# Kernel tuning notes

Hardware: AMD Instinct MI355X
Metric: run time of the kernel (lower is better)

## Reference

```python
import jax, jax.numpy as jnp
import numpy as np


def setup_inputs() -> dict:
    key = jax.random.key(0)
    k1, k2 = jax.random.split(key)
    T, D, E = 8192, 4096, 64
    x = jax.random.normal(k1, (T, D), dtype=jnp.float32)
    gate_w = jax.random.normal(k2, (E, D), dtype=jnp.float32) * (1.0 / np.sqrt(D))
    return {"x": x, "gate_w": gate_w}


def reference(x, gate_w):
    TOPK = 8
    # logits = x @ W^T, computed in float32 like .float() in torch
    logits = jnp.einsum('td,ed->te', x, gate_w).astype(jnp.float32)
    scores = jax.nn.sigmoid(scores_in := logits) if False else jax.nn.sigmoid(logits)
    # top-k scores per token; values are exactly the gathered weights
    weights, indices = jax.lax.top_k(scores, TOPK)
    weights = weights / jnp.clip(jnp.sum(weights, axis=-1, keepdims=True), 1e-12)
    return weights.astype(x.dtype), indices
```

## Files before the change

### kernel.cpp

```cpp
#include <hip/hip_runtime.h>
#include <math.h>

#define T_TOTAL 8192
#define D_TOTAL 4096
#define E 64
#define TOPK 8
#define NKB (D_TOTAL / 32)

typedef short short8 __attribute__((ext_vector_type(8)));
typedef float f32x4 __attribute__((ext_vector_type(4)));

__device__ __forceinline__ void split3(const float* v8, short8& h, short8& m, short8& l) {
#pragma unroll
    for (int j = 0; j < 8; ++j) {
        const float f = v8[j];
        const unsigned u = __float_as_uint(f);
        const unsigned hu = u & 0xffff0000u;
        const float r1 = f - __uint_as_float(hu);
        const unsigned mu = __float_as_uint(r1) & 0xffff0000u;
        const float r2 = r1 - __uint_as_float(mu);
        const unsigned lu = __float_as_uint(r2);
        h[j] = (short)(hu >> 16);
        m[j] = (short)(mu >> 16);
        l[j] = (short)(lu >> 16);
    }
}

__device__ __forceinline__ void split3v(const float* v, short8& h, short8& m, short8& l) {
    unsigned* hp = reinterpret_cast<unsigned*>(&h);
    unsigned* mp = reinterpret_cast<unsigned*>(&m);
    unsigned* lp = reinterpret_cast<unsigned*>(&l);
#pragma unroll
    for (int p = 0; p < 4; ++p) {
        const float a = v[2 * p], b = v[2 * p + 1];
        const unsigned hw = __builtin_amdgcn_perm(__float_as_uint(b), __float_as_uint(a), 0x07060302u);
        const float r0 = a - __uint_as_float(hw << 16);
        const float r1 = b - __uint_as_float(hw & 0xffff0000u);
        const unsigned mw = __builtin_amdgcn_perm(__float_as_uint(r1), __float_as_uint(r0), 0x07060302u);
        const float s0 = r0 - __uint_as_float(mw << 16);
        const float s1 = r1 - __uint_as_float(mw & 0xffff0000u);
        const unsigned lw = __builtin_amdgcn_perm(__float_as_uint(s1), __float_as_uint(s0), 0x07060302u);
        hp[p] = hw; mp[p] = mw; lp[p] = lw;
    }
}

__global__ __launch_bounds__(256)
void prep_w(const float* __restrict__ w, short8* __restrict__ Bh,
            short8* __restrict__ Bm, short8* __restrict__ Bl) {
    const int t = blockIdx.x * 256 + threadIdx.x;
    const int lane = t & 63;
    const int nt = (t >> 6) & 3;
    const int kb = t >> 8;
    const int e = nt * 16 + (lane & 15);
    const int k = kb * 32 + (lane >> 4) * 8;

    const float* src = w + (size_t)e * D_TOTAL + k;
    float v[8];
    *reinterpret_cast<float4*>(&v[0]) = *reinterpret_cast<const float4*>(src);
    *reinterpret_cast<float4*>(&v[4]) = *reinterpret_cast<const float4*>(src + 4);

    short8 h, m, l;
    split3(v, h, m, l);
    Bh[t] = h; Bm[t] = m; Bl[t] = l;
}

__global__ __launch_bounds__(1024, 8)
void fused_router(const float* __restrict__ x,
                  const short8* __restrict__ Bh, const short8* __restrict__ Bm,
                  const short8* __restrict__ Bl,
                  float* __restrict__ out) {
    __shared__ float tiles[8 * 1024];
    __shared__ float fin[1024];

    const int tid = threadIdx.x;
    const int lane = tid & 63;
    const int wv = tid >> 6;
    const int tok0 = blockIdx.x * 16;

    const int row = lane & 15;
    const int kq = lane >> 4;

    const float* xb = x + (size_t)(tok0 + row) * D_TOTAL + kq * 8;

    f32x4 acc[4];
#pragma unroll
    for (int n = 0; n < 4; ++n) acc[n] = (f32x4){0.f, 0.f, 0.f, 0.f};

    const int kbase = wv * 256;

    float xr[8];
    {
        const float* ap = xb + kbase;
        *reinterpret_cast<float4*>(&xr[0]) = *reinterpret_cast<const float4*>(ap);
        *reinterpret_cast<float4*>(&xr[4]) = *reinterpret_cast<const float4*>(ap + 4);
    }

#pragma unroll
    for (int kb = 0; kb < 8; ++kb) {
        const int k = kbase + kb * 32;
        const int gkb = k >> 5;

        short8 ah, am_, al;
        split3v(xr, ah, am_, al);
        if (kb < 7) {
            const float* ap = xb + k + 32;
            *reinterpret_cast<float4*>(&xr[0]) = *reinterpret_cast<const float4*>(ap);
            *reinterpret_cast<float4*>(&xr[4]) = *reinterpret_cast<const float4*>(ap + 4);
        }

#pragma unroll
        for (int nt = 0; nt < 4; ++nt) {
            const size_t bi = (size_t)(gkb * 4 + nt) * 64 + lane;
            const short8 bh = Bh[bi];
            const short8 bm = Bm[bi];
            const short8 bl = Bl[bi];
            f32x4 c = acc[nt];
            c = __builtin_amdgcn_mfma_f32_16x16x32_bf16(ah,  bh, c, 0, 0, 0);
            c = __builtin_amdgcn_mfma_f32_16x16x32_bf16(ah,  bm, c, 0, 0, 0);
            c = __builtin_amdgcn_mfma_f32_16x16x32_bf16(am_, bh, c, 0, 0, 0);
            c = __builtin_amdgcn_mfma_f32_16x16x32_bf16(am_, bm, c, 0, 0, 0);
            c = __builtin_amdgcn_mfma_f32_16x16x32_bf16(ah,  bl, c, 0, 0, 0);
            c = __builtin_amdgcn_mfma_f32_16x16x32_bf16(al,  bh, c, 0, 0, 0);
            acc[nt] = c;
        }
    }

    if (wv >= 8) {
        float* s = &tiles[(size_t)(wv - 8) * 1024 + lane];
#pragma unroll
        for (int nt = 0; nt < 4; ++nt)
#pragma unroll
            for (int r = 0; r < 4; ++r)
                s[(nt * 4 + r) * 64] = acc[nt][r];
    }
    __syncthreads();
    if (wv < 8) {
        float* s = &tiles[(size_t)wv * 1024 + lane];
#pragma unroll
        for (int nt = 0; nt < 4; ++nt)
#pragma unroll
            for (int r = 0; r < 4; ++r) {
                const int j = (nt * 4 + r) * 64;
                s[j] = acc[nt][r] + s[j];
            }
    }
    __syncthreads();

    {
        float s0 = 0.f;
#pragma unroll
        for (int w2 = 0; w2 < 8; ++w2) s0 += tiles[w2 * 1024 + tid];
        const int j = tid >> 6, ln = tid & 63;
        const int t = (ln >> 4) * 4 + (j & 3);
        const int e = (j >> 2) * 16 + (ln & 15);
        fin[t * 64 + e] = s0;
    }
    __syncthreads();

    {
        const int t = wv;
        float v = fin[t * 64 + lane];
        float wj[TOPK];
        int   ij[TOPK];
        float wsum = 0.f;
#pragma unroll
        for (int j = 0; j < TOPK; ++j) {
            float mx = v;
#pragma unroll
            for (int off = 32; off >= 1; off >>= 1)
                mx = fmaxf(mx, __shfl_xor(mx, off));
            const unsigned long long msk = __ballot(v == mx);
            const int widx = (int)__builtin_ctzll(msk);
            wj[j] = 1.f / (1.f + expf(-mx));
            ij[j] = widx;
            wsum += wj[j];
            if (lane == widx) v = -INFINITY;
        }
        const float inv = 1.f / fmaxf(wsum, 1e-12f);
        const int tg = tok0 + t;
        if (lane == 0) {
#pragma unroll
            for (int j = 0; j < TOPK; ++j)
                out[(size_t)tg * TOPK + j] = wj[j] * inv;
#pragma unroll
            for (int j = 0; j < TOPK; ++j)
                out[(size_t)T_TOTAL * TOPK + (size_t)tg * TOPK + j] = (float)ij[j];
        }
    }
}

extern "C" void kernel_launch(void* const* d_in, const int* in_sizes, int n_in,
                              void* d_out, int out_size, void* d_ws, size_t ws_size,
                              hipStream_t stream) {
    const float* x = (const float*)d_in[0];
    const float* w = (const float*)d_in[1];
    float* out = (float*)d_out;

    short8* Bh = (short8*)d_ws;
    short8* Bm = Bh + (size_t)NKB * 4 * 64;
    short8* Bl = Bm + (size_t)NKB * 4 * 64;

    prep_w<<<NKB * 4 * 64 / 256, 256, 0, stream>>>(w, Bh, Bm, Bl);
    fused_router<<<T_TOTAL / 16, 1024, 0, stream>>>(x, Bh, Bm, Bl, out);
}
```

Before: 58.74 us.

## Split-K GEMM with LDS-staged weights and separate top-k reduction kernel

Replaces the fused per-16-token kernel with a split-K GEMM. Each block loads one K-chunk of the pre-split bf16 weight planes into LDS and reuses it across 256 tokens, with x loads triple-buffered. Partial logits are written to a workspace and then summed by a new top-k kernel that also runs sigmoid, selection and normalization. This cuts redundant global weight reads across token blocks, at the cost of an extra launch and about 32MB of partial-sum traffic.

```diff
diff --git a/kernel.cpp b/kernel.cpp
--- a/kernel.cpp
+++ b/kernel.cpp
@@ -6,6 +6,14 @@
 #define E 64
 #define TOPK 8
 #define NKB (D_TOTAL / 32)
+
+#define S_SPLIT 16
+#define KCH (D_TOTAL / S_SPLIT)
+#define KB_PER_BLK (KCH / 32)
+#define TOKW 16
+#define WVS 16
+#define TOKB (TOKW * WVS)
+#define CHUNK8 (KB_PER_BLK * 4 * 64)
 
 typedef short short8 __attribute__((ext_vector_type(8)));
 typedef float f32x4 __attribute__((ext_vector_type(4)));
@@ -64,101 +72,125 @@
     Bh[t] = h; Bm[t] = m; Bl[t] = l;
 }
 
-__global__ __launch_bounds__(1024, 8)
-void fused_router(const float* __restrict__ x,
-                  const short8* __restrict__ Bh, const short8* __restrict__ Bm,
-                  const short8* __restrict__ Bl,
-                  float* __restrict__ out) {
-    __shared__ float tiles[8 * 1024];
-    __shared__ float fin[1024];
+__global__ __launch_bounds__(1024, 4)
+void gemm_lds(const float* __restrict__ x,
+              const short8* __restrict__ Bh, const short8* __restrict__ Bm,
+              const short8* __restrict__ Bl,
+              float* __restrict__ part) {
+    __shared__ short8 Bs[3 * CHUNK8];
 
     const int tid = threadIdx.x;
     const int lane = tid & 63;
     const int wv = tid >> 6;
-    const int tok0 = blockIdx.x * 16;
+    const int s = blockIdx.y;
+    const int tok0 = blockIdx.x * TOKB + wv * TOKW;
+
+    {
+        const short8* g0 = Bh + (size_t)s * CHUNK8;
+        const short8* g1 = Bm + (size_t)s * CHUNK8;
+        const short8* g2 = Bl + (size_t)s * CHUNK8;
+#pragma unroll
+        for (int t = 0; t < 6; ++t) {
+            const int j = t * 1024 + tid;
+            const int a = j >> 11;
+            const int idx = j & (CHUNK8 - 1);
+            const short8* g = (a == 0) ? g0 : (a == 1) ? g1 : g2;
+            Bs[j] = g[idx];
+        }
+    }
 
     const int row = lane & 15;
     const int kq = lane >> 4;
-
-    const float* xb = x + (size_t)(tok0 + row) * D_TOTAL + kq * 8;
+    const float* xb = x + (size_t)(tok0 + row) * D_TOTAL + s * KCH + kq * 8;
 
     f32x4 acc[4];
 #pragma unroll
     for (int n = 0; n < 4; ++n) acc[n] = (f32x4){0.f, 0.f, 0.f, 0.f};
 
-    const int kbase = wv * 256;
-
-    float xr[8];
-    {
-        const float* ap = xb + kbase;
-        *reinterpret_cast<float4*>(&xr[0]) = *reinterpret_cast<const float4*>(ap);
-        *reinterpret_cast<float4*>(&xr[4]) = *reinterpret_cast<const float4*>(ap + 4);
-    }
-
-#pragma unroll
-    for (int kb = 0; kb < 8; ++kb) {
-        const int k = kbase + kb * 32;
-        const int gkb = k >> 5;
+    float xr[3][8];
+#pragma unroll
+    for (int p = 0; p < 2; ++p) {
+        const float* ap = xb + p * 32;
+        *reinterpret_cast<float4*>(&xr[p][0]) = *reinterpret_cast<const float4*>(ap);
+        *reinterpret_cast<float4*>(&xr[p][4]) = *reinterpret_cast<const float4*>(ap + 4);
+    }
+
+    __syncthreads();
+
+#pragma unroll
+    for (int kb = 0; kb < KB_PER_BLK; ++kb) {
+        if (kb < KB_PER_BLK - 2) {
+            const float* ap = xb + (kb + 2) * 32;
+            *reinterpret_cast<float4*>(&xr[(kb + 2) % 3][0]) = *reinterpret_cast<const float4*>(ap);
+            *reinterpret_cast<float4*>(&xr[(kb + 2) % 3][4]) = *reinterpret_cast<const float4*>(ap + 4);
+        }
 
         short8 ah, am_, al;
-        split3v(xr, ah, am_, al);
-        if (kb < 7) {
-            const float* ap = xb + k + 32;
-            *reinterpret_cast<float4*>(&xr[0]) = *reinterpret_cast<const float4*>(ap);
-            *reinterpret_cast<float4*>(&xr[4]) = *reinterpret_cast<const float4*>(ap + 4);
-        }
-
+        split3v(xr[kb % 3], ah, am_, al);
+
+        short8 bh[4], bm[4], bl[4];
 #pragma unroll
         for (int nt = 0; nt < 4; ++nt) {
-            const size_t bi = (size_t)(gkb * 4 + nt) * 64 + lane;
-            const short8 bh = Bh[bi];
-            const short8 bm = Bm[bi];
-            const short8 bl = Bl[bi];
+            const int bi = (kb * 4 + nt) * 64 + lane;
+            bh[nt] = Bs[bi];
+            bm[nt] = Bs[CHUNK8 + bi];
+            bl[nt] = Bs[2 * CHUNK8 + bi];
+        }
+
+#pragma unroll
+        for (int nt = 0; nt < 4; ++nt) {
             f32x4 c = acc[nt];
-            c = __builtin_amdgcn_mfma_f32_16x16x32_bf16(ah,  bh, c, 0, 0, 0);
-            c = __builtin_amdgcn_mfma_f32_16x16x32_bf16(ah,  bm, c, 0, 0, 0);
-            c = __builtin_amdgcn_mfma_f32_16x16x32_bf16(am_, bh, c, 0, 0, 0);
-            c = __builtin_amdgcn_mfma_f32_16x16x32_bf16(am_, bm, c, 0, 0, 0);
-            c = __builtin_amdgcn_mfma_f32_16x16x32_bf16(ah,  bl, c, 0, 0, 0);
-            c = __builtin_amdgcn_mfma_f32_16x16x32_bf16(al,  bh, c, 0, 0, 0);
+            c = __builtin_amdgcn_mfma_f32_16x16x32_bf16(ah,  bh[nt], c, 0, 0, 0);
+            c = __builtin_amdgcn_mfma_f32_16x16x32_bf16(ah,  bm[nt], c, 0, 0, 0);
+            c = __builtin_amdgcn_mfma_f32_16x16x32_bf16(am_, bh[nt], c, 0, 0, 0);
+            c = __builtin_amdgcn_mfma_f32_16x16x32_bf16(am_, bm[nt], c, 0, 0, 0);
+            c = __builtin_amdgcn_mfma_f32_16x16x32_bf16(ah,  bl[nt], c, 0, 0, 0);
+            c = __builtin_amdgcn_mfma_f32_16x16x32_bf16(al,  bh[nt], c, 0, 0, 0);
             acc[nt] = c;
         }
     }
 
-    if (wv >= 8) {
-        float* s = &tiles[(size_t)(wv - 8) * 1024 + lane];
-#pragma unroll
-        for (int nt = 0; nt < 4; ++nt)
-#pragma unroll
-            for (int r = 0; r < 4; ++r)
-                s[(nt * 4 + r) * 64] = acc[nt][r];
-    }
+    float* pb = part + ((size_t)s * T_TOTAL + tok0) * E;
+#pragma unroll
+    for (int nt = 0; nt < 4; ++nt) {
+        const int e = nt * 16 + (lane & 15);
+#pragma unroll
+        for (int r = 0; r < 4; ++r) {
+            const int t = (lane >> 4) * 4 + r;
+            pb[(size_t)t * E + e] = acc[nt][r];
+        }
+    }
+}
+
+__global__ __launch_bounds__(256)
+void topk_kernel(const float* __restrict__ part, float* __restrict__ out) {
+    __shared__ float fin[32 * 64];
+
+    const int tid = threadIdx.x;
+    const int tok0 = blockIdx.x * 32;
+    const size_t base = (size_t)tok0 * E;
+
+    const int f = tid * 8;
+    float4 v0 = make_float4(0.f, 0.f, 0.f, 0.f);
+    float4 v1 = make_float4(0.f, 0.f, 0.f, 0.f);
+#pragma unroll
+    for (int s = 0; s < S_SPLIT; ++s) {
+        const float4* p = reinterpret_cast<const float4*>(
+            part + (size_t)s * T_TOTAL * E + base + f);
+        const float4 a = p[0];
+        const float4 b = p[1];
+        v0.x += a.x; v0.y += a.y; v0.z += a.z; v0.w += a.w;
+        v1.x += b.x; v1.y += b.y; v1.z += b.z; v1.w += b.w;
+    }
+    *reinterpret_cast<float4*>(&fin[f]) = v0;
+    *reinterpret_cast<float4*>(&fin[f + 4]) = v1;
     __syncthreads();
-    if (wv < 8) {
-        float* s = &tiles[(size_t)wv * 1024 + lane];
-#pragma unroll
-        for (int nt = 0; nt < 4; ++nt)
-#pragma unroll
-            for (int r = 0; r < 4; ++r) {
-                const int j = (nt * 4 + r) * 64;
-                s[j] = acc[nt][r] + s[j];
-            }
-    }
-    __syncthreads();
-
-    {
-        float s0 = 0.f;
-#pragma unroll
-        for (int w2 = 0; w2 < 8; ++w2) s0 += tiles[w2 * 1024 + tid];
-        const int j = tid >> 6, ln = tid & 63;
-        const int t = (ln >> 4) * 4 + (j & 3);
-        const int e = (j >> 2) * 16 + (ln & 15);
-        fin[t * 64 + e] = s0;
-    }
-    __syncthreads();
-
-    {
-        const int t = wv;
+
+    const int lane = tid & 63;
+    const int wv = tid >> 6;
+#pragma unroll
+    for (int rep = 0; rep < 8; ++rep) {
+        const int t = wv * 8 + rep;
         float v = fin[t * 64 + lane];
         float wj[TOPK];
         int   ij[TOPK];
@@ -196,10 +228,13 @@
     const float* w = (const float*)d_in[1];
     float* out = (float*)d_out;
 
-    short8* Bh = (short8*)d_ws;
+    float* part = (float*)d_ws;
+    short8* Bh = (short8*)((char*)d_ws + (size_t)S_SPLIT * T_TOTAL * E * sizeof(float));
     short8* Bm = Bh + (size_t)NKB * 4 * 64;
     short8* Bl = Bm + (size_t)NKB * 4 * 64;
 
     prep_w<<<NKB * 4 * 64 / 256, 256, 0, stream>>>(w, Bh, Bm, Bl);
-    fused_router<<<T_TOTAL / 16, 1024, 0, stream>>>(x, Bh, Bm, Bl, out);
-}
+    dim3 g(T_TOTAL / TOKB, S_SPLIT);
+    gemm_lds<<<g, 1024, 0, stream>>>(x, Bh, Bm, Bl, part);
+    topk_kernel<<<T_TOTAL / 32, 256, 0, stream>>>(part, out);
+}
```

Result: slower. 69.69 us (+18.6%).
